# Optimization experiments

Hardware: AMD Instinct MI355X
Metric: run time of the kernel (lower is better)

## Reference

```python
import math
import jax
import jax.numpy as jnp
import numpy as np

KS = 7  # kernel_size


def _make_cdt_kernel():
    # kornia.create_meshgrid(k,k,normalized=False) -> coords; centered; hypot -> exp(d/-0.35)
    r = np.arange(KS, dtype=np.float32) - (KS // 2)
    yy, xx = np.meshgrid(r, r, indexing="ij")
    k = np.exp(np.hypot(xx, yy) / -0.35)
    return jnp.asarray(k, jnp.float32)[None, None]  # (1,1,KS,KS) OIHW


def setup_inputs() -> dict:
    key = jax.random.key(0)
    B, C, H, W = 32, 3, 256, 256
    u = jax.random.uniform(key, (B, C, H, W), dtype=jnp.float32)
    image = (u < 0.005).astype(jnp.float32)
    return {"image": image}


def reference(image):
    B, C, H, W = image.shape
    kernel = _make_cdt_kernel()
    n_iters = math.ceil(max(H, W) / (KS // 2))  # static
    x = image.reshape(B * C, 1, H, W)
    out0 = jnp.zeros_like(x)

    def step(carry, i):
        out, boundary = carry
        conv = jax.lax.conv_general_dilated(
            boundary, kernel, (1, 1), "SAME",
            dimension_numbers=("NCHW", "OIHW", "NCHW"))
        # -0.35*log(conv) with posinf (conv==0) replaced by 0, exactly as
        # torch.nan_to_num(cdt, posinf=0.0); safe-log form avoids inf/nan.
        pos = conv > 0
        cdt = jnp.where(pos, -0.35 * jnp.log(jnp.where(pos, conv, 1.0)), 0.0)
        mask = cdt > 0
        offset = i.astype(jnp.float32) * (KS / 2)  # i * kernel_size / 2 (true div)
        out = out + jnp.where(mask, offset + cdt, 0.0)
        boundary = jnp.where(mask, 1.0, boundary)
        return (out, boundary), None

    (out, _), _ = jax.lax.scan(step, (out0, x), jnp.arange(n_iters))
    return out.reshape(B, C, H, W)
```

## Files before the change

kernel.cpp:

```cpp
#include <hip/hip_runtime.h>


typedef unsigned short u16x4 __attribute__((ext_vector_type(4)));

#define BIGV (1 << 20)
#define ROWB 272
#define CHB (256 * ROWB)

__global__ __launch_bounds__(256) void k_rowdist(const float* __restrict__ img,
                                                 unsigned char* __restrict__ d1) {
  const int lane = threadIdx.x & 63;
  const int wv = threadIdx.x >> 6;
  const int nwg = (int)gridDim.x;
  const int o = (int)blockIdx.x;
  const int l = (o & 7) * (nwg >> 3) + (o >> 3);
  const int row = l * 4 + wv;
  const int x0 = lane * 4;

  const float4 v = *reinterpret_cast<const float4*>(&img[(size_t)row * 256 + x0]);

  int c0 = (v.x != 0.0f) ? -x0 : BIGV;
  int c1 = (v.y != 0.0f) ? -(x0 + 1) : BIGV;
  int c2 = (v.z != 0.0f) ? -(x0 + 2) : BIGV;
  int c3 = (v.w != 0.0f) ? -(x0 + 3) : BIGV;
  const int p0 = c0;
  const int p1 = min(c1, p0);
  const int p2 = min(c2, p1);
  const int p3 = min(c3, p2);
  int incl = p3;
#pragma unroll
  for (int off = 1; off < 64; off <<= 1) {
    int o2 = __shfl_up(incl, off, 64);
    if (lane >= off) incl = min(incl, o2);
  }
  int excl = __shfl_up(incl, 1, 64);
  if (lane == 0) excl = BIGV;
  const int df0 = x0 + min(p0, excl);
  const int df1 = x0 + 1 + min(p1, excl);
  const int df2 = x0 + 2 + min(p2, excl);
  const int df3 = x0 + 3 + min(p3, excl);

  int g0 = (v.x != 0.0f) ? x0 : BIGV;
  int g1 = (v.y != 0.0f) ? (x0 + 1) : BIGV;
  int g2 = (v.z != 0.0f) ? (x0 + 2) : BIGV;
  int g3 = (v.w != 0.0f) ? (x0 + 3) : BIGV;
  const int q3 = g3;
  const int q2 = min(g2, q3);
  const int q1 = min(g1, q2);
  const int q0 = min(g0, q1);
  int incl2 = q0;
#pragma unroll
  for (int off = 1; off < 64; off <<= 1) {
    int o2 = __shfl_down(incl2, off, 64);
    if (lane < 64 - off) incl2 = min(incl2, o2);
  }
  int excl2 = __shfl_down(incl2, 1, 64);
  if (lane == 63) excl2 = BIGV;
  const int db0 = min(q0, excl2) - x0;
  const int db1 = min(q1, excl2) - (x0 + 1);
  const int db2 = min(q2, excl2) - (x0 + 2);
  const int db3 = min(q3, excl2) - (x0 + 3);

  const unsigned int d0 = (unsigned int)min(min(df0, db0), 127);
  const unsigned int d1v = (unsigned int)min(min(df1, db1), 127);
  const unsigned int d2 = (unsigned int)min(min(df2, db2), 127);
  const unsigned int d3 = (unsigned int)min(min(df3, db3), 127);
  const int ch = row >> 8, y = row & 255;
  const size_t base = (size_t)ch * CHB + (size_t)y * ROWB;
  *reinterpret_cast<unsigned int*>(&d1[base + 8 + x0]) =
      d0 | (d1v << 8) | (d2 << 16) | (d3 << 24);
  if (lane < 2)
    *reinterpret_cast<unsigned int*>(&d1[base + lane * 4]) = 0u;
  else if (lane >= 62)
    *reinterpret_cast<unsigned int*>(&d1[base + 264 + (lane - 62) * 4]) = 0u;
}

#define LDQ(off) (*reinterpret_cast<const u16x4*>(&s1[(off)]))
#define EMIN __builtin_elementwise_min
#define EMAX __builtin_elementwise_max

#define IND(q_, CP) ((((q_) + (CP)) & 0x80808080u) >> 7)

#define PT0(s_)                                                                 \
  aD##s_ += IND(q0, Cp##s_); aD##s_ += IND(q1, Cp##s_);                         \
  aC##s_ += IND(q2, Cp##s_); aC##s_ += IND(q3, Cp##s_);                         \
  aC##s_ += IND(q4, Cp##s_); aD##s_ += IND(q5, Cp##s_);                         \
  aD##s_ += IND(q6, Cp##s_);
#define PT1(s_)                                                                 \
  aD##s_ += IND(q0, Cp##s_); aC##s_ += IND(q1, Cp##s_);                         \
  aB##s_ += IND(q2, Cp##s_); aB##s_ += IND(q3, Cp##s_);                         \
  aB##s_ += IND(q4, Cp##s_); aC##s_ += IND(q5, Cp##s_);                         \
  aD##s_ += IND(q6, Cp##s_);
#define PT2(s_)                                                                 \
  aC##s_ += IND(q0, Cp##s_); aB##s_ += IND(q1, Cp##s_);                         \
  aA##s_ += IND(q2, Cp##s_); aA##s_ += IND(q3, Cp##s_);                         \
  aA##s_ += IND(q4, Cp##s_); aB##s_ += IND(q5, Cp##s_);                         \
  aC##s_ += IND(q6, Cp##s_);
#define PT3(s_)                                   \
  aC##s_ += IND(q0, Cp##s_); aB##s_ += IND(q1, Cp##s_);                         \
  aA##s_ += IND(q2, Cp##s_);                                                    \
  aA##s_ += IND(q4, Cp##s_); aB##s_ += IND(q5, Cp##s_);                         \
  aC##s_ += IND(q6, Cp##s_);

#define ROWU(u_, ...)                                                           \
  do {                                                                          \
    const unsigned char* pu_ = &Ds[(rl0 + (u_)) * 44 + jb2];                    \
    const unsigned int R0_ = *reinterpret_cast<const unsigned int*>(pu_);       \
    const unsigned int R1_ = *reinterpret_cast<const unsigned int*>(pu_ + 4);   \
    const unsigned int R2_ = *reinterpret_cast<const unsigned int*>(pu_ + 8);   \
    const unsigned int q0 = __builtin_amdgcn_alignbyte(R1_, R0_, 1);            \
    const unsigned int q1 = __builtin_amdgcn_alignbyte(R1_, R0_, 2);            \
    const unsigned int q2 = __builtin_amdgcn_alignbyte(R1_, R0_, 3);            \
    const unsigned int q3 = R1_;                                                \
    const unsigned int q4 = __builtin_amdgcn_alignbyte(R2_, R1_, 1);            \
    const unsigned int q5 = __builtin_amdgcn_alignbyte(R2_, R1_, 2);            \
    const unsigned int q6 = __builtin_amdgcn_alignbyte(R2_, R1_, 3);            \
    (void)q0; (void)q1; (void)q2; (void)q3; (void)q4; (void)q5; (void)q6;       \
    __VA_ARGS__                                                                 \
  } while (0)

#define CPSET(s_, DC)                                                           \
  const unsigned int Cp##s_ =                                                   \
      (unsigned int)(127 - 3 * ((max((int)((DC)&255u) - 1, 0) * 86) >> 8)) |    \
      ((unsigned int)(127 - 3 * ((max((int)(((DC) >> 8) & 255u) - 1, 0) * 86) >> 8)) << 8) | \
      ((unsigned int)(127 - 3 * ((max((int)(((DC) >> 16) & 255u) - 1, 0) * 86) >> 8)) << 16) | \
      ((unsigned int)(127 - 3 * ((max((int)((DC) >> 24) - 1, 0) * 86) >> 8)) << 24)

#define FIN(s_, DC)                                                             \
  do {                                                                          \
    const int d0_ = (int)((DC)&255u);                                           \
    const int d1_ = (int)(((DC) >> 8) & 255u);                                  \
    const int d2_ = (int)(((DC) >> 16) & 255u);                                 \
    const int d3_ = (int)((DC) >> 24);                                          \
    const int i0_ = (max(d0_ - 1, 0) * 86) >> 8;                                \
    const int i1_ = (max(d1_ - 1, 0) * 86) >> 8;                                \
    const int i2_ = (max(d2_ - 1, 0) * 86) >> 8;                                \
    const int i3_ = (max(d3_ - 1, 0) * 86) >> 8;                                \
    const float s0_ = fmaf((float)(aA##s_ & 255u), wA,                          \
                     fmaf((float)(aB##s_ & 255u), wB,                           \
                     fmaf((float)(aC##s_ & 255u), wC,                           \
                          (float)(aD##s_ & 255u) * wD)));                       \
    const float s1_ = fmaf((float)((aA##s_ >> 8) & 255u), wA,                   \
                     fmaf((float)((aB##s_ >> 8) & 255u), wB,                    \
                     fmaf((float)((aC##s_ >> 8) & 255u), wC,                    \
                          (float)((aD##s_ >> 8) & 255u) * wD)));                \
    const float s2_ = fmaf((float)((aA##s_ >> 16) & 255u), wA,                  \
                     fmaf((float)((aB##s_ >> 16) & 255u), wB,                   \
                     fmaf((float)((aC##s_ >> 16) & 255u), wC,                   \
                          (float)((aD##s_ >> 16) & 255u) * wD)));               \
    const float s3_ = fmaf((float)(aA##s_ >> 24), wA,                           \
                     fmaf((float)(aB##s_ >> 24), wB,                            \
                     fmaf((float)(aC##s_ >> 24), wC,                            \
                          (float)(aD##s_ >> 24) * wD)));                        \
    const float cv0_ = W4 - s0_, cv1_ = W4 - s1_;                               \
    const float cv2_ = W4 - s2_, cv3_ = W4 - s3_;                               \
    const float e0_ = fmaf(3.5f, (float)i0_, -0.35f * __logf(fmaxf(cv0_, 1e-30f))); \
    const float e1_ = fmaf(3.5f, (float)i1_, -0.35f * __logf(fmaxf(cv1_, 1e-30f))); \
    const float e2_ = fmaf(3.5f, (float)i2_, -0.35f * __logf(fmaxf(cv2_, 1e-30f))); \
    const float e3_ = fmaf(3.5f, (float)i3_, -0.35f * __logf(fmaxf(cv3_, 1e-30f))); \
    const float4 o4_ = make_float4(                                             \
        (d0_ > 0 && cv0_ > 1e-6f) ? e0_ : 0.0f,                                 \
        (d1_ > 0 && cv1_ > 1e-6f) ? e1_ : 0.0f,                                 \
        (d2_ > 0 && cv2_ > 1e-6f) ? e2_ : 0.0f,                                 \
        (d3_ > 0 && cv3_ > 1e-6f) ? e3_ : 0.0f);                                \
    *reinterpret_cast<float4*>(&out[obase + (size_t)(s_) * 256]) = o4_;         \
  } while (0)

__global__ __launch_bounds__(256) void k_fused(const unsigned char* __restrict__ d1,
                                               float* __restrict__ out) {
  const int nwg = (int)gridDim.x;
  const int o = (int)blockIdx.x;
  const int l = (o & 7) * (nwg >> 3) + (o >> 3);
  const int xt = l & 7;
  const int yt = (l >> 3) & 1;
  const int ch = l >> 4;
  const int x0 = xt * 32;
  const int y0 = yt * 128;
  const int tid = threadIdx.x;
  const int lastxt = 7;

  __shared__ __align__(16) unsigned char s1[256 * 96];
  __shared__ __align__(16) unsigned char Ds[134 * 44];

  const unsigned char* src = d1 + (size_t)ch * CHB + x0;
#pragma unroll
  for (int it = 0; it < 3; ++it) {
    const int idx = it * 256 + tid;
    const int y = (idx * 21846) >> 16;
    const int seg = idx - y * 3;
    const uint4 q = *reinterpret_cast<const uint4*>(&src[y * ROWB + seg * 16]);
    uint4 lo, hi;
    lo.x = __builtin_amdgcn_perm(0u, q.x, 0x0C010C00u);
    lo.y = __builtin_amdgcn_perm(0u, q.x, 0x0C030C02u);
    lo.z = __builtin_amdgcn_perm(0u, q.y, 0x0C010C00u);
    lo.w = __builtin_amdgcn_perm(0u, q.y, 0x0C030C02u);
    hi.x = __builtin_amdgcn_perm(0u, q.z, 0x0C010C00u);
    hi.y = __builtin_amdgcn_perm(0u, q.z, 0x0C030C02u);
    hi.z = __builtin_amdgcn_perm(0u, q.w, 0x0C010C00u);
    hi.w = __builtin_amdgcn_perm(0u, q.w, 0x0C030C02u);
    *reinterpret_cast<uint4*>(&s1[y * 96 + seg * 32]) = lo;
    *reinterpret_cast<uint4*>(&s1[y * 96 + seg * 32 + 16]) = hi;
  }
  __syncthreads();

  const u16x4 K1 = {1, 1, 1, 1}, K2 = {2, 2, 2, 2}, K3 = {3, 3, 3, 3},
              K4 = {4, 4, 4, 4}, K5 = {5, 5, 5, 5}, K6 = {6, 6, 6, 6},
              K7 = {7, 7, 7, 7}, K8 = {8, 8, 8, 8};
#pragma unroll 1
  for (int it = 0; it < 6; ++it) {
    const int idx = it * 256 + tid;
    if (idx >= 1340) break;
    const int r = (idx * 6554) >> 16;
    const int g = idx - r * 10;
    const int y = y0 + r - 3;
    const bool ghost =
        (xt == 0 && g == 0) || (xt == lastxt && g == 9) || y < 0 || y > 255;
    if (ghost) {
      *reinterpret_cast<unsigned int*>(&Ds[r * 44 + g * 4]) = 0x7F7F7F7Fu;
      continue;
    }
    const int jb = 8 + 8 * g;
    const int rb = y * 96 + jb;
    const int bot = 255 * 96 + jb;
    const u16x4 b0 = LDQ(rb);
    const u16x4 u1 = LDQ(max(rb - 96, jb));
    const u16x4 u2 = LDQ(max(rb - 192, jb));
    const u16x4 u3 = LDQ(max(rb - 288, jb));
    const u16x4 u4 = LDQ(max(rb - 384, jb));
    const u16x4 u5 = LDQ(max(rb - 480, jb));
    const u16x4 u6 = LDQ(max(rb - 576, jb));
    const u16x4 u7 = LDQ(max(rb - 672, jb));
    const u16x4 u8 = LDQ(max(rb - 768, jb));
    const u16x4 w1 = LDQ(min(rb + 96, bot));
    const u16x4 w2 = LDQ(min(rb + 192, bot));
    const u16x4 w3 = LDQ(min(rb + 288, bot));
    const u16x4 w4 = LDQ(min(rb + 384, bot));
    const u16x4 w5 = LDQ(min(rb + 480, bot));
    const u16x4 w6 = LDQ(min(rb + 576, bot));
    const u16x4 w7 = LDQ(min(rb + 672, bot));
    const u16x4 w8 = LDQ(min(rb + 768, bot));
    const u16x4 mu = EMIN(EMIN(EMIN(EMAX(u1, K1), EMAX(u2, K2)),
                                EMIN(EMAX(u3, K3), EMAX(u4, K4))),
                          EMIN(EMIN(EMAX(u5, K5), EMAX(u6, K6)),
                                EMIN(EMAX(u7, K7), EMAX(u8, K8))));
    const u16x4 mw = EMIN(EMIN(EMIN(EMAX(w1, K1), EMAX(w2, K2)),
                                EMIN(EMAX(w3, K3), EMAX(w4, K4))),
                          EMIN(EMIN(EMAX(w5, K5), EMAX(w6, K6)),
                                EMIN(EMAX(w7, K7), EMAX(w8, K8))));
    u16x4 b = EMIN(b0, EMIN(mu, mw));
    unsigned long long bb = __builtin_bit_cast(unsigned long long, b);
    unsigned int blo = (unsigned int)bb, bhi = (unsigned int)(bb >> 32);
    int bm = max(max((int)(blo & 0xFFFFu), (int)(blo >> 16)),
                 max((int)(bhi & 0xFFFFu), (int)(bhi >> 16)));
    int k = 9;
    int au = rb - 768, ad = rb + 768;
    while (k < bm) {
      const unsigned short t1 = (unsigned short)k, t2 = (unsigned short)(k + 1),
                           t3 = (unsigned short)(k + 2), t4 = (unsigned short)(k + 3);
      const u16x4 c1 = {t1, t1, t1, t1}, c2 = {t2, t2, t2, t2},
                  c3 = {t3, t3, t3, t3}, c4 = {t4, t4, t4, t4};
      const u16x4 a1 = LDQ(max(au - 96, jb));
      const u16x4 a2 = LDQ(max(au - 192, jb));
      const u16x4 a3 = LDQ(max(au - 288, jb));
      const u16x4 a4 = LDQ(max(au - 384, jb));
      const u16x4 e1 = LDQ(min(ad + 96, bot));
      const u16x4 e2 = LDQ(min(ad + 192, bot));
      const u16x4 e3 = LDQ(min(ad + 288, bot));
      const u16x4 e4 = LDQ(min(ad + 384, bot));
      const u16x4 t = EMIN(EMIN(EMIN(EMAX(a1, c1), EMAX(a2, c2)),
                                 EMIN(EMAX(a3, c3), EMAX(a4, c4))),
                           EMIN(EMIN(EMAX(e1, c1), EMAX(e2, c2)),
                                 EMIN(EMAX(e3, c3), EMAX(e4, c4))));
      b = EMIN(b, t);
      au -= 384;
      ad += 384;
      k += 4;
      bb = __builtin_bit_cast(unsigned long long, b);
      blo = (unsigned int)bb;
      bhi = (unsigned int)(bb >> 32);
      bm = max(max((int)(blo & 0xFFFFu), (int)(blo >> 16)),
               max((int)(bhi & 0xFFFFu), (int)(bhi >> 16)));
    }
    const unsigned int packed = __builtin_amdgcn_perm(bhi, blo, 0x06040200u);
    *reinterpret_cast<unsigned int*>(&Ds[r * 44 + g * 4]) = packed;
  }
  __syncthreads();

  const float wA = 3.17814e-2f, wB = 2.35426e-3f, wC = 1.91126e-4f, wD = 1.35150e-5f;
  const float W4 = 8.0f * wA + 12.0f * wB + 16.0f * wC + 12.0f * wD;

  const int cg = tid & 7;
  const int rg = tid >> 3;
  const int rl0 = rg * 4;
  const int jb2 = cg * 4;
  const size_t obase = (size_t)ch * 65536 + (size_t)(y0 + rl0) * 256 + x0 + cg * 4;

  const unsigned int Dc0 =
      *reinterpret_cast<const unsigned int*>(&Ds[(rl0 + 3) * 44 + jb2 + 4]);
  const unsigned int Dc1 =
      *reinterpret_cast<const unsigned int*>(&Ds[(rl0 + 4) * 44 + jb2 + 4]);
  const unsigned int Dc2 =
      *reinterpret_cast<const unsigned int*>(&Ds[(rl0 + 5) * 44 + jb2 + 4]);
  const unsigned int Dc3 =
      *reinterpret_cast<const unsigned int*>(&Ds[(rl0 + 6) * 44 + jb2 + 4]);
  CPSET(0, Dc0);
  CPSET(1, Dc1);
  CPSET(2, Dc2);
  CPSET(3, Dc3);

  unsigned int aA0 = 0, aB0 = 0, aC0 = 0, aD0 = 0;
  unsigned int aA1 = 0, aB1 = 0, aC1 = 0, aD1 = 0;
  unsigned int aA2 = 0, aB2 = 0, aC2 = 0, aD2 = 0;
  unsigned int aA3 = 0, aB3 = 0, aC3 = 0, aD3 = 0;

  ROWU(0, PT0(0));
  ROWU(1, PT1(0) PT0(1));
  ROWU(2, PT2(0) PT1(1) PT0(2));
  ROWU(3, PT3(0) PT2(1) PT1(2) PT0(3));
  ROWU(4, PT2(0) PT3(1) PT2(2) PT1(3));
  ROWU(5, PT1(0) PT2(1) PT3(2) PT2(3));
  ROWU(6, PT0(0) PT1(1) PT2(2) PT3(3));
  ROWU(7, PT0(1) PT1(2) PT2(3));
  ROWU(8, PT0(2) PT1(3));
  ROWU(9, PT0(3));

  FIN(0, Dc0);
  FIN(1, Dc1);
  FIN(2, Dc2);
  FIN(3, Dc3);
}

extern "C" void kernel_launch(void* const* d_in, const int* in_sizes, int n_in,
                              void* d_out, int out_size, void* d_ws, size_t ws_size,
                              hipStream_t stream) {
  const float* img = (const float*)d_in[0];
  float* out = (float*)d_out;
  unsigned char* Dbuf = (unsigned char*)d_ws;

  const int total = in_sizes[0];
  const int nch = total >> 16;

  k_rowdist<<<dim3(nch * 64), dim3(256), 0, stream>>>(img, Dbuf);
  k_fused<<<dim3(nch * 16), dim3(256), 0, stream>>>(Dbuf, out);
}
```

Before: 43.43 us.

## Process full-height column strips per workgroup instead of half-height tiles

Each k_fused workgroup now covers all 256 rows of a 32-column strip instead of 128 rows, halving the grid and giving each thread 8 output rows instead of 4. This removes the duplicated s1 staging and the 6-row vertical halo that two half-tiles both computed, and lets each Ds row feed more outputs. The cost is a larger shared-memory Ds buffer, more registers per thread (accumulators for 8 rows), and only half as many workgroups to fill the GPU.

```diff
diff --git a/kernel.cpp b/kernel.cpp
--- a/kernel.cpp
+++ b/kernel.cpp
@@ -172,15 +172,13 @@
   const int o = (int)blockIdx.x;
   const int l = (o & 7) * (nwg >> 3) + (o >> 3);
   const int xt = l & 7;
-  const int yt = (l >> 3) & 1;
-  const int ch = l >> 4;
+  const int ch = l >> 3;
   const int x0 = xt * 32;
-  const int y0 = yt * 128;
   const int tid = threadIdx.x;
   const int lastxt = 7;
 
   __shared__ __align__(16) unsigned char s1[256 * 96];
-  __shared__ __align__(16) unsigned char Ds[134 * 44];
+  __shared__ __align__(16) unsigned char Ds[262 * 44];
 
   const unsigned char* src = d1 + (size_t)ch * CHB + x0;
 #pragma unroll
@@ -207,12 +205,12 @@
               K4 = {4, 4, 4, 4}, K5 = {5, 5, 5, 5}, K6 = {6, 6, 6, 6},
               K7 = {7, 7, 7, 7}, K8 = {8, 8, 8, 8};
 #pragma unroll 1
-  for (int it = 0; it < 6; ++it) {
+  for (int it = 0; it < 11; ++it) {
     const int idx = it * 256 + tid;
-    if (idx >= 1340) break;
+    if (idx >= 2620) break;
     const int r = (idx * 6554) >> 16;
     const int g = idx - r * 10;
-    const int y = y0 + r - 3;
+    const int y = r - 3;
     const bool ghost =
         (xt == 0 && g == 0) || (xt == lastxt && g == 9) || y < 0 || y > 255;
     if (ghost) {
@@ -291,9 +289,9 @@
 
   const int cg = tid & 7;
   const int rg = tid >> 3;
-  const int rl0 = rg * 4;
+  const int rl0 = rg * 8;
   const int jb2 = cg * 4;
-  const size_t obase = (size_t)ch * 65536 + (size_t)(y0 + rl0) * 256 + x0 + cg * 4;
+  const size_t obase = (size_t)ch * 65536 + (size_t)rl0 * 256 + x0 + cg * 4;
 
   const unsigned int Dc0 =
       *reinterpret_cast<const unsigned int*>(&Ds[(rl0 + 3) * 44 + jb2 + 4]);
@@ -303,31 +301,48 @@
       *reinterpret_cast<const unsigned int*>(&Ds[(rl0 + 5) * 44 + jb2 + 4]);
   const unsigned int Dc3 =
       *reinterpret_cast<const unsigned int*>(&Ds[(rl0 + 6) * 44 + jb2 + 4]);
-  CPSET(0, Dc0);
-  CPSET(1, Dc1);
-  CPSET(2, Dc2);
-  CPSET(3, Dc3);
+  const unsigned int Dc4 =
+      *reinterpret_cast<const unsigned int*>(&Ds[(rl0 + 7) * 44 + jb2 + 4]);
+  const unsigned int Dc5 =
+      *reinterpret_cast<const unsigned int*>(&Ds[(rl0 + 8) * 44 + jb2 + 4]);
+  const unsigned int Dc6 =
+      *reinterpret_cast<const unsigned int*>(&Ds[(rl0 + 9) * 44 + jb2 + 4]);
+  const unsigned int Dc7 =
+      *reinterpret_cast<const unsigned int*>(&Ds[(rl0 + 10) * 44 + jb2 + 4]);
+  CPSET(0, Dc0); CPSET(1, Dc1); CPSET(2, Dc2); CPSET(3, Dc3);
+  CPSET(4, Dc4); CPSET(5, Dc5); CPSET(6, Dc6); CPSET(7, Dc7);
 
   unsigned int aA0 = 0, aB0 = 0, aC0 = 0, aD0 = 0;
   unsigned int aA1 = 0, aB1 = 0, aC1 = 0, aD1 = 0;
   unsigned int aA2 = 0, aB2 = 0, aC2 = 0, aD2 = 0;
   unsigned int aA3 = 0, aB3 = 0, aC3 = 0, aD3 = 0;
+  unsigned int aA4 = 0, aB4 = 0, aC4 = 0, aD4 = 0;
+  unsigned int aA5 = 0, aB5 = 0, aC5 = 0, aD5 = 0;
+  unsigned int aA6 = 0, aB6 = 0, aC6 = 0, aD6 = 0;
+  unsigned int aA7 = 0, aB7 = 0, aC7 = 0, aD7 = 0;
 
   ROWU(0, PT0(0));
   ROWU(1, PT1(0) PT0(1));
   ROWU(2, PT2(0) PT1(1) PT0(2));
   ROWU(3, PT3(0) PT2(1) PT1(2) PT0(3));
-  ROWU(4, PT2(0) PT3(1) PT2(2) PT1(3));
-  ROWU(5, PT1(0) PT2(1) PT3(2) PT2(3));
-  ROWU(6, PT0(0) PT1(1) PT2(2) PT3(3));
-  ROWU(7, PT0(1) PT1(2) PT2(3));
-  ROWU(8, PT0(2) PT1(3));
-  ROWU(9, PT0(3));
-
+  ROWU(4, PT2(0) PT3(1) PT2(2) PT1(3) PT0(4));
+  ROWU(5, PT1(0) PT2(1) PT3(2) PT2(3) PT1(4) PT0(5));
+  ROWU(6, PT0(0) PT1(1) PT2(2) PT3(3) PT2(4) PT1(5) PT0(6));
   FIN(0, Dc0);
+  ROWU(7, PT0(1) PT1(2) PT2(3) PT3(4) PT2(5) PT1(6) PT0(7));
   FIN(1, Dc1);
+  ROWU(8, PT0(2) PT1(3) PT2(4) PT3(5) PT2(6) PT1(7));
   FIN(2, Dc2);
+  ROWU(9, PT0(3) PT1(4) PT2(5) PT3(6) PT2(7));
   FIN(3, Dc3);
+  ROWU(10, PT0(4) PT1(5) PT2(6) PT3(7));
+  FIN(4, Dc4);
+  ROWU(11, PT0(5) PT1(6) PT2(7));
+  FIN(5, Dc5);
+  ROWU(12, PT0(6) PT1(7));
+  FIN(6, Dc6);
+  ROWU(13, PT0(7));
+  FIN(7, Dc7);
 }
 
 extern "C" void kernel_launch(void* const* d_in, const int* in_sizes, int n_in,
@@ -341,5 +356,5 @@
   const int nch = total >> 16;
 
   k_rowdist<<<dim3(nch * 64), dim3(256), 0, stream>>>(img, Dbuf);
-  k_fused<<<dim3(nch * 16), dim3(256), 0, stream>>>(Dbuf, out);
+  k_fused<<<dim3(nch * 8), dim3(256), 0, stream>>>(Dbuf, out);
 }
```

Measured after the change: 44.10 us. No clear change (+1.5%).
